# Optimization experiments

Hardware: AMD Instinct MI355X
Metric: run time of the kernel (lower is better)

## Reference

```python
import jax, jax.numpy as jnp
import numpy as np

PATCH = 3      # patch_size = (3, 3)
STRIDE = 1     # filter_patch_stride == compare_stride == 1
EPS = 1e-12    # F.normalize eps


def extract_patches(x, ph, pw, stride):
    """x: (B, C, H, W) -> (B, nH*nW, C, ph, pw), valid patches."""
    B, C, H, W = x.shape
    oh = (H - ph) // stride + 1
    ow = (W - pw) // stride + 1
    rows = (jnp.arange(oh) * stride)[:, None] + jnp.arange(ph)[None, :]  # (oh, ph)
    cols = (jnp.arange(ow) * stride)[:, None] + jnp.arange(pw)[None, :]  # (ow, pw)
    # gather -> (B, C, oh, ph, ow, pw)
    p = x[:, :, rows[:, :, None, None], cols[None, None, :, :]]
    return p.transpose(0, 2, 4, 1, 3, 5).reshape(B, oh * ow, C, ph, pw)


def l2norm(x, axis):
    # matches F.normalize(p=2): x / max(||x||, eps)
    return x / jnp.maximum(jnp.linalg.norm(x, axis=axis, keepdims=True), EPS)


def setup_inputs() -> dict:
    key = jax.random.key(0)
    k1, k2 = jax.random.split(key)
    pred_style = jax.random.normal(k1, (4, 256, 64, 64), dtype=jnp.float32)
    target_style = jax.random.normal(k2, (4, 256, 64, 64), dtype=jnp.float32)
    return {"pred_style": pred_style, "target_style": target_style}


def reference(pred_style, target_style):
    # patches of the raw (unnormalized) features
    tp = extract_patches(target_style, PATCH, PATCH, STRIDE)   # (B, nP, C, ph, pw)
    pp = extract_patches(pred_style, PATCH, PATCH, STRIDE)     # (B, nP, C, ph, pw)

    # best_match: normalize content feature over channels, style patches over channel dim (dim=2)
    x1n = l2norm(pred_style, axis=1)
    tpn = l2norm(tp, axis=2)
    x1p = extract_patches(x1n, PATCH, PATCH, STRIDE)           # (B, nP, C, ph, pw)

    # conv-as-cosine-correlation == batched patch dot products, then argmax over style patches
    scores = jnp.einsum('bqcij,bpcij->bqp', x1p, tpn)          # (B, nP, nP)
    match = jnp.argmax(scores, axis=2)                         # (B, nP)

    # gather best-matching target patches (indices detached in original via .data)
    new_t = jnp.take_along_axis(tp, match[:, :, None, None, None], axis=1)
    return jnp.mean((pp - new_t) ** 2)
```

## Files before the change

kernel.cpp:

```cpp
#include <hip/hip_runtime.h>
#include <hip/hip_bf16.h>

#define NB 4
#define CH 256
#define HH 64
#define WW 64
#define NPIX 4096
#define OH 62
#define NPATCH 3844
#define KDIM 256
#define EPSN 1e-12f
#define VSTRIDE 65

typedef __attribute__((ext_vector_type(8))) short short8;
typedef __attribute__((ext_vector_type(4))) float f32x4;

__device__ __forceinline__ float bf16_to_f32(unsigned short u) {
    return __uint_as_float((unsigned)u << 16);
}
__device__ __forceinline__ unsigned short f32_to_bf16(float f) {
    __hip_bfloat16 h = __float2bfloat16(f);
    return *(unsigned short*)&h;
}

__global__ __launch_bounds__(256) void k_prep(const float* __restrict__ pred,
                                              const float* __restrict__ tgt,
                                              __hip_bfloat16* __restrict__ Xn,
                                              __hip_bfloat16* __restrict__ Tn,
                                              float* __restrict__ ssP, float* __restrict__ invP,
                                              float* __restrict__ ssT, float* __restrict__ invT,
                                              unsigned long long* __restrict__ keys,
                                              float* __restrict__ out) {
    const int bz = blockIdx.y;
    const int b = bz >> 1, which = bz & 1;
    const float* src = (which ? tgt : pred) + (size_t)b * CH * NPIX;
    unsigned short* dst = (unsigned short*)((which ? Tn : Xn) + (size_t)b * NPIX * CH);
    float* ss_g  = (which ? ssT  : ssP)  + b * NPIX;
    float* inv_g = (which ? invT : invP) + b * NPIX;
    const int pix0 = blockIdx.x * 64;
    const int t = threadIdx.x, lane = t & 63, wv = t >> 6;

    int gid = (bz * 64 + blockIdx.x) * 256 + t;
    if (gid < NB * NPATCH) keys[gid] = 0ull;
    if (gid == 0) out[0] = 0.f;

    __shared__ unsigned short stage[CH][65];
    __shared__ float partial[4][64];
    __shared__ float inv_s[64];

    float ssacc = 0.f;
#pragma unroll 8
    for (int cc = 0; cc < 64; ++cc) {
        int c = wv * 64 + cc;
        float v = src[(size_t)c * NPIX + pix0 + lane];
        ssacc += v * v;
        stage[c][lane] = f32_to_bf16(v);
    }
    partial[wv][lane] = ssacc;
    __syncthreads();
    if (t < 64) {
        float ss = partial[0][t] + partial[1][t] + partial[2][t] + partial[3][t];
        float inv = 1.f / fmaxf(sqrtf(ss), EPSN);
        ss_g[pix0 + t] = ss;
        inv_g[pix0 + t] = inv;
        inv_s[t] = inv;
    }
    __syncthreads();
    for (int p = wv; p < 64; p += 4) {
        float iv = inv_s[p];
#pragma unroll
        for (int cb = 0; cb < 4; ++cb) {
            int c = cb * 64 + lane;
            float v = bf16_to_f32(stage[c][p]) * iv;
            dst[(size_t)(pix0 + p) * CH + c] = f32_to_bf16(v);
        }
    }
}

__device__ __forceinline__ void gload_lds16(const void* g, void* l) {
    __builtin_amdgcn_global_load_lds(
        (const __attribute__((address_space(1))) void*)g,
        (__attribute__((address_space(3))) void*)l, 16, 0, 0);
}

__global__ __launch_bounds__(256) void k_gemm(const __hip_bfloat16* __restrict__ A,
                                              const __hip_bfloat16* __restrict__ Bm,
                                              unsigned short* __restrict__ Dout) {
    __shared__ short As[128 * 32];
    __shared__ short Bs[128 * 32];
    const int z = blockIdx.z;
    const int t = threadIdx.x;
    const int lane = t & 63, wv = t >> 6;
    const int wm = wv >> 1, wn = wv & 1;
    const int row0 = blockIdx.y * 128, col0 = blockIdx.x * 128;
    const short* Ag = (const short*)A + (size_t)z * NPIX * CH;
    const short* Bg = (const short*)Bm + (size_t)z * NPIX * CH;
    unsigned short* D = Dout + (size_t)z * NPIX * NPIX;
    const int srow = t >> 2;
    const int kch  = (t & 3) * 8;

    f32x4 acc[4][4] = {};

    for (int k0 = 0; k0 < KDIM; k0 += 32) {
        gload_lds16(Ag + (size_t)(row0 + srow) * KDIM + k0 + kch,      As + wv * 512);
        gload_lds16(Ag + (size_t)(row0 + 64 + srow) * KDIM + k0 + kch, As + 2048 + wv * 512);
        gload_lds16(Bg + (size_t)(col0 + srow) * KDIM + k0 + kch,      Bs + wv * 512);
        gload_lds16(Bg + (size_t)(col0 + 64 + srow) * KDIM + k0 + kch, Bs + 2048 + wv * 512);
        __syncthreads();

        const int rsel = lane & 15, ksel = (lane >> 4) * 8;
        short8 a[4], bfr[4];
#pragma unroll
        for (int mi = 0; mi < 4; ++mi)
            a[mi] = *(const short8*)&As[(wm * 64 + mi * 16 + rsel) * 32 + ksel];
#pragma unroll
        for (int ni = 0; ni < 4; ++ni)
            bfr[ni] = *(const short8*)&Bs[(wn * 64 + ni * 16 + rsel) * 32 + ksel];
#pragma unroll
        for (int mi = 0; mi < 4; ++mi)
#pragma unroll
            for (int ni = 0; ni < 4; ++ni)
                acc[mi][ni] = __builtin_amdgcn_mfma_f32_16x16x32_bf16(a[mi], bfr[ni], acc[mi][ni], 0, 0, 0);
        __syncthreads();
    }
    const int rbase = (lane >> 4) * 4, cbase = lane & 15;
#pragma unroll
    for (int mi = 0; mi < 4; ++mi) {
#pragma unroll
        for (int ni = 0; ni < 4; ++ni) {
            int r0 = row0 + wm * 64 + mi * 16 + rbase;
            int c  = col0 + wn * 64 + ni * 16 + cbase;
#pragma unroll
            for (int r = 0; r < 4; ++r)
                D[(size_t)(r0 + r) * NPIX + c] = f32_to_bf16(acc[mi][ni][r]);
        }
    }
}

__global__ __launch_bounds__(256) void k_score(const unsigned short* __restrict__ Dbase,
                                               unsigned long long* __restrict__ keys) {
    const int z = blockIdx.z;
    const unsigned short* D = Dbase + (size_t)z * NPIX * NPIX;
    const int pr = blockIdx.x, qr = blockIdx.y;
    const int t = threadIdx.x;

    __shared__ float VT[64 * VSTRIDE + 8];

    const int a  = t >> 2;
    const int b0 = (t & 3) * 16;
    float v[16];
#pragma unroll
    for (int e = 0; e < 16; ++e) v[e] = 0.f;
#pragma unroll
    for (int i = 0; i < 3; ++i) {
        const unsigned short* rp =
            D + (size_t)((qr + i) * 64 + a) * NPIX + (pr + i) * 64 + b0;
        uint4 u0 = *(const uint4*)rp;
        uint4 u1 = *(const uint4*)(rp + 8);
        const unsigned* uw = (const unsigned*)&u0;
#pragma unroll
        for (int w = 0; w < 4; ++w) {
            v[2 * w]     += bf16_to_f32((unsigned short)uw[w]);
            v[2 * w + 1] += bf16_to_f32((unsigned short)(uw[w] >> 16));
        }
        const unsigned* uw1 = (const unsigned*)&u1;
#pragma unroll
        for (int w = 0; w < 4; ++w) {
            v[8 + 2 * w]     += bf16_to_f32((unsigned short)uw1[w]);
            v[8 + 2 * w + 1] += bf16_to_f32((unsigned short)(uw1[w] >> 16));
        }
    }
#pragma unroll
    for (int e = 0; e < 16; ++e)
        VT[(b0 + e) * VSTRIDE + a] = v[e];
    __syncthreads();

    const int g = t >> 6, qc = t & 63;
    float best = -1e30f; int bpc = 0;
    const int kmax = (g == 3) ? 14 : 16;
    for (int k = 0; k < kmax; ++k) {
        int pc = g * 16 + k;
        float s = VT[pc * VSTRIDE + qc]
                + VT[(pc + 1) * VSTRIDE + qc + 1]
                + VT[(pc + 2) * VSTRIDE + qc + 2];
        if (s > best) { best = s; bpc = pc; }
    }
    if (qc < OH) {
        unsigned u = __float_as_uint(best);
        u = (best >= 0.f) ? (u | 0x80000000u) : ~u;
        unsigned long long key = ((unsigned long long)u << 12)
                               | (unsigned)((63 - pr) << 6) | (unsigned)(63 - bpc);
        atomicMax(&keys[(size_t)z * NPATCH + qr * OH + qc], key);
    }
}

__global__ void k_loss(const unsigned short* __restrict__ Dbase,
                       const unsigned long long* __restrict__ keys,
                       const float* __restrict__ ssPb, const float* __restrict__ invPb,
                       const float* __restrict__ ssTb, const float* __restrict__ invTb,
                       float* __restrict__ out) {
    const int z = blockIdx.y;
    const unsigned short* D = Dbase + (size_t)z * NPIX * NPIX;
    const float* ssP  = ssPb  + z * NPIX;
    const float* invP = invPb + z * NPIX;
    const float* ssT  = ssTb  + z * NPIX;
    const float* invT = invTb + z * NPIX;
    int q = blockIdx.x * 256 + threadIdx.x;
    float acc = 0.f;
    if (q < NPATCH) {
        int qr = q / OH, qc = q - qr * OH;
        int qpix = qr * WW + qc;
        unsigned long long key = keys[(size_t)z * NPATCH + q];
        int mpr = 63 - (int)((key >> 6) & 63);
        int mpc = 63 - (int)(key & 63);
        int mpix = mpr * WW + mpc;
#pragma unroll
        for (int i = 0; i < 3; ++i)
#pragma unroll
            for (int j = 0; j < 3; ++j) {
                int off = i * WW + j;
                int y = qpix + off, x = mpix + off;
                float Dv = bf16_to_f32(D[(size_t)y * NPIX + x]);
                float nP = ssP[y] * invP[y];
                float nT = ssT[x] * invT[x];
                acc += ssP[y] + ssT[x] - 2.f * Dv * nP * nT;
            }
    }
#pragma unroll
    for (int s = 32; s > 0; s >>= 1) acc += __shfl_down(acc, s, 64);
    if ((threadIdx.x & 63) == 0)
        atomicAdd(out, acc * (1.f / 35426304.f));
}

extern "C" void kernel_launch(void* const* d_in, const int* in_sizes, int n_in,
                              void* d_out, int out_size, void* d_ws, size_t ws_size,
                              hipStream_t stream) {
    const float* pred = (const float*)d_in[0];
    const float* tgt  = (const float*)d_in[1];
    char* ws = (char*)d_ws;
    unsigned short*     Dws  = (unsigned short*)(ws);
    __hip_bfloat16*     Xn   = (__hip_bfloat16*)(ws + 134217728);
    __hip_bfloat16*     Tn   = (__hip_bfloat16*)(ws + 142606336);
    float*              ssP  = (float*)(ws + 150994944);
    float*              invP = (float*)(ws + 151060480);
    float*              ssT  = (float*)(ws + 151126016);
    float*              invT = (float*)(ws + 151191552);
    unsigned long long* keys = (unsigned long long*)(ws + 151257088);

    k_prep<<<dim3(64, 8), 256, 0, stream>>>(pred, tgt, Xn, Tn, ssP, invP, ssT, invT,
                                            keys, (float*)d_out);
    k_gemm<<<dim3(32, 32, 4), 256, 0, stream>>>(Xn, Tn, Dws);
    k_score<<<dim3(62, 62, 4), 256, 0, stream>>>(Dws, keys);
    k_loss<<<dim3(16, 4), 256, 0, stream>>>(Dws, keys, ssP, invP, ssT, invT,
                                            (float*)d_out);
}
```

Before: 204.6 us.

## Process two diagonal-adjacent row pairs per score block to reuse loaded tiles

```diff
diff --git a/kernel.cpp b/kernel.cpp
--- a/kernel.cpp
+++ b/kernel.cpp
@@ -10,7 +10,7 @@
 #define NPATCH 3844
 #define KDIM 256
 #define EPSN 1e-12f
-#define VSTRIDE 65
+#define VROW 68
 
 typedef __attribute__((ext_vector_type(8))) short short8;
 typedef __attribute__((ext_vector_type(4))) float f32x4;
@@ -137,60 +137,96 @@
     }
 }
 
+__device__ __forceinline__ void load_tile16(const unsigned short* __restrict__ D,
+                                            int row, int col, float* f) {
+    const unsigned short* rp = D + (size_t)row * NPIX + col;
+    uint4 u0 = *(const uint4*)rp;
+    uint4 u1 = *(const uint4*)(rp + 8);
+    const unsigned* w0 = (const unsigned*)&u0;
+    const unsigned* w1 = (const unsigned*)&u1;
+#pragma unroll
+    for (int w = 0; w < 4; ++w) {
+        f[2 * w]         = bf16_to_f32((unsigned short)w0[w]);
+        f[2 * w + 1]     = bf16_to_f32((unsigned short)(w0[w] >> 16));
+        f[8 + 2 * w]     = bf16_to_f32((unsigned short)w1[w]);
+        f[8 + 2 * w + 1] = bf16_to_f32((unsigned short)(w1[w] >> 16));
+    }
+}
+
 __global__ __launch_bounds__(256) void k_score(const unsigned short* __restrict__ Dbase,
                                                unsigned long long* __restrict__ keys) {
     const int z = blockIdx.z;
+    const int dg = (int)blockIdx.x - 61;
+    const int adg = dg < 0 ? -dg : dg;
+    const int len = 62 - adg;
+    const int s0 = blockIdx.y * 2;
+    if (s0 >= len) return;
+    const bool two = (s0 + 1 < len);
+    const int qr = (dg > 0 ? dg : 0) + s0;
+    const int pr = qr - dg;
     const unsigned short* D = Dbase + (size_t)z * NPIX * NPIX;
-    const int pr = blockIdx.x, qr = blockIdx.y;
     const int t = threadIdx.x;
 
-    __shared__ float VT[64 * VSTRIDE + 8];
-
-    const int a  = t >> 2;
-    const int b0 = (t & 3) * 16;
-    float v[16];
-#pragma unroll
-    for (int e = 0; e < 16; ++e) v[e] = 0.f;
-#pragma unroll
-    for (int i = 0; i < 3; ++i) {
-        const unsigned short* rp =
-            D + (size_t)((qr + i) * 64 + a) * NPIX + (pr + i) * 64 + b0;
-        uint4 u0 = *(const uint4*)rp;
-        uint4 u1 = *(const uint4*)(rp + 8);
-        const unsigned* uw = (const unsigned*)&u0;
-#pragma unroll
-        for (int w = 0; w < 4; ++w) {
-            v[2 * w]     += bf16_to_f32((unsigned short)uw[w]);
-            v[2 * w + 1] += bf16_to_f32((unsigned short)(uw[w] >> 16));
-        }
-        const unsigned* uw1 = (const unsigned*)&u1;
-#pragma unroll
-        for (int w = 0; w < 4; ++w) {
-            v[8 + 2 * w]     += bf16_to_f32((unsigned short)uw1[w]);
-            v[8 + 2 * w + 1] += bf16_to_f32((unsigned short)(uw1[w] >> 16));
-        }
-    }
-#pragma unroll
-    for (int e = 0; e < 16; ++e)
-        VT[(b0 + e) * VSTRIDE + a] = v[e];
+    __shared__ __align__(16) float V[2][64 * VROW];
+
+    const int a = t >> 2, b0 = (t & 3) * 16;
+    {
+        float acc0[16], acc1[16], f[16];
+        load_tile16(D, (qr + 0) * 64 + a, (pr + 0) * 64 + b0, f);
+#pragma unroll
+        for (int e = 0; e < 16; ++e) acc0[e] = f[e];
+        load_tile16(D, (qr + 1) * 64 + a, (pr + 1) * 64 + b0, f);
+#pragma unroll
+        for (int e = 0; e < 16; ++e) { acc0[e] += f[e]; acc1[e] = f[e]; }
+        load_tile16(D, (qr + 2) * 64 + a, (pr + 2) * 64 + b0, f);
+#pragma unroll
+        for (int e = 0; e < 16; ++e) { acc0[e] += f[e]; acc1[e] += f[e]; }
+#pragma unroll
+        for (int e = 0; e < 16; e += 4)
+            *(f32x4*)&V[0][a * VROW + b0 + e] = *(const f32x4*)&acc0[e];
+        if (two) {
+            load_tile16(D, (qr + 3) * 64 + a, (pr + 3) * 64 + b0, f);
+#pragma unroll
+            for (int e = 0; e < 16; ++e) acc1[e] += f[e];
+#pragma unroll
+            for (int e = 0; e < 16; e += 4)
+                *(f32x4*)&V[1][a * VROW + b0 + e] = *(const f32x4*)&acc1[e];
+        }
+    }
     __syncthreads();
 
     const int g = t >> 6, qc = t & 63;
-    float best = -1e30f; int bpc = 0;
+    const int qcr = qc < OH ? qc : (OH - 1);
+    const int pc0 = g * 16;
     const int kmax = (g == 3) ? 14 : 16;
-    for (int k = 0; k < kmax; ++k) {
-        int pc = g * 16 + k;
-        float s = VT[pc * VSTRIDE + qc]
-                + VT[(pc + 1) * VSTRIDE + qc + 1]
-                + VT[(pc + 2) * VSTRIDE + qc + 2];
-        if (s > best) { best = s; bpc = pc; }
-    }
-    if (qc < OH) {
-        unsigned u = __float_as_uint(best);
-        u = (best >= 0.f) ? (u | 0x80000000u) : ~u;
-        unsigned long long key = ((unsigned long long)u << 12)
-                               | (unsigned)((63 - pr) << 6) | (unsigned)(63 - bpc);
-        atomicMax(&keys[(size_t)z * NPATCH + qr * OH + qc], key);
+    const int npair = two ? 2 : 1;
+    for (int pp = 0; pp < npair; ++pp) {
+        const float* Vb = V[pp];
+        float r0[16], r1[20], r2[20];
+#pragma unroll
+        for (int e = 0; e < 16; e += 4)
+            *(f32x4*)&r0[e] = *(const f32x4*)&Vb[qcr * VROW + pc0 + e];
+#pragma unroll
+        for (int e = 0; e < 20; e += 4)
+            *(f32x4*)&r1[e] = *(const f32x4*)&Vb[(qcr + 1) * VROW + pc0 + e];
+#pragma unroll
+        for (int e = 0; e < 20; e += 4)
+            *(f32x4*)&r2[e] = *(const f32x4*)&Vb[(qcr + 2) * VROW + pc0 + e];
+        float best = -1e30f; int bpc = 0;
+#pragma unroll
+        for (int k = 0; k < 16; ++k) {
+            if (k >= kmax) break;
+            float s = r0[k] + r1[k + 1] + r2[k + 2];
+            if (s > best) { best = s; bpc = pc0 + k; }
+        }
+        if (qc < OH) {
+            unsigned u = __float_as_uint(best);
+            u = (best >= 0.f) ? (u | 0x80000000u) : ~u;
+            unsigned long long key = ((unsigned long long)u << 12)
+                                   | (unsigned)((63 - (pr + pp)) << 6)
+                                   | (unsigned)(63 - bpc);
+            atomicMax(&keys[(size_t)z * NPATCH + (qr + pp) * OH + qc], key);
+        }
     }
 }
 
@@ -250,7 +286,7 @@
     k_prep<<<dim3(64, 8), 256, 0, stream>>>(pred, tgt, Xn, Tn, ssP, invP, ssT, invT,
                                             keys, (float*)d_out);
     k_gemm<<<dim3(32, 32, 4), 256, 0, stream>>>(Xn, Tn, Dws);
-    k_score<<<dim3(62, 62, 4), 256, 0, stream>>>(Dws, keys);
+    k_score<<<dim3(123, 31, 4), 256, 0, stream>>>(Dws, keys);
     k_loss<<<dim3(16, 4), 256, 0, stream>>>(Dws, keys, ssP, invP, ssT, invT,
                                             (float*)d_out);
 }
```

New measurement: 211.7 us. 1.03x slower.
